# Kernel tuning notes

Hardware: AMD Instinct MI355X
Metric: run time of the kernel (lower is better)

## Reference

```python
import jax, jax.numpy as jnp
import numpy as np

EPS = 1e-6        # RMSNorm140 eps
LAM = 0.1         # lambda_: second-order score weight
HAD = 0.05        # hadamard_scale

def _rmsnorm(x, w):
    return x * jax.lax.rsqrt(jnp.mean(x * x, axis=-1, keepdims=True) + EPS) * w

def _rope(x):
    # x: [b, h, s, d]; interleaved-pair rotary embedding (theta=10000)
    b, h, s, d = x.shape
    inv = 1.0 / (10000.0 ** (jnp.arange(0, d, 2, dtype=jnp.float32) / d))
    ang = jnp.arange(s, dtype=jnp.float32)[:, None] * inv[None, :]  # [s, d/2]
    cos, sin = jnp.cos(ang), jnp.sin(ang)
    x1, x2 = x[..., 0::2], x[..., 1::2]
    out = jnp.stack([x1 * cos - x2 * sin, x1 * sin + x2 * cos], axis=-1)
    return out.reshape(b, h, s, d)

def _rotate_half(x):
    d = x.shape[-1] // 2
    return jnp.concatenate([-x[..., d:], x[..., :d]], axis=-1)

def _attn_pass(Q, K, V):
    # scores = (Q@K^T + lam * Q^2 @ (K^2)^T) / sqrt(head_dim)   (second-order amplify)
    scale = 1.0 / jnp.sqrt(jnp.float32(Q.shape[-1]))
    scores = (jnp.einsum('bhsd,bhtd->bhst', Q, K)
              + LAM * jnp.einsum('bhsd,bhtd->bhst', Q * Q, K * K)) * scale
    return jnp.einsum('bhst,bhtd->bhsd', jax.nn.softmax(scores, axis=-1), V)

def _attention(x, wq, wk, wv, wo, gate_w):
    b, s, dim = x.shape
    hd = gate_w.shape[0]
    nh = dim // hd
    def proj(w):  # StickyLinear: x @ W^T, W stored [out, in]
        return (x @ w.T).reshape(b, s, nh, hd).transpose(0, 2, 1, 3)  # [b,h,s,d]
    Q, K, V = proj(wq), proj(wk), proj(wv)
    Q, K = _rope(Q), _rope(K)
    out1 = _attn_pass(Q, K, V)
    # rotated second pass + per-channel sigmoid gate over head_dim
    out2 = _attn_pass(_rotate_half(Q), _rotate_half(K), V)
    g = jax.nn.sigmoid(gate_w)
    out = out1 * (1.0 - g) + out2 * g
    out = out + HAD * out * out  # Hadamard mix (elementwise nonlinearity)
    out = out.transpose(0, 2, 1, 3).reshape(b, s, dim)
    return out @ wo.T

def _ffn(x, w1, w3, w2):
    # SwiGLU: down( silu(gate(x)) * up(x) )
    return (jax.nn.silu(x @ w1.T) * (x @ w3.T)) @ w2.T

def reference(x, norm1_w, norm2_w, wq, wk, wv, wo, gate_w, w1, w3, w2):
    h = x + _attention(_rmsnorm(x, norm1_w), wq, wk, wv, wo, gate_w)
    return h + _ffn(_rmsnorm(h, norm2_w), w1, w3, w2)

def setup_inputs() -> dict:
    B, S, D, NH, DFF = 2, 1024, 2048, 16, 8192
    HD = D // NH
    key = jax.random.key(0)
    ks = jax.random.split(key, 9)
    std = 0.02
    return {
        'x': jax.random.normal(ks[0], (B, S, D), dtype=jnp.float32),
        'norm1_w': jnp.ones((D,), jnp.float32),
        'norm2_w': jnp.ones((D,), jnp.float32),
        'wq': jax.random.normal(ks[1], (D, D), jnp.float32) * std,
        'wk': jax.random.normal(ks[2], (D, D), jnp.float32) * std,
        'wv': jax.random.normal(ks[3], (D, D), jnp.float32) * std,
        'wo': jax.random.normal(ks[4], (D, D), jnp.float32) * std,
        'gate_w': jax.random.normal(ks[5], (HD,), jnp.float32) * 0.01,
        'w1': jax.random.normal(ks[6], (DFF, D), jnp.float32) * std,
        'w3': jax.random.normal(ks[7], (DFF, D), jnp.float32) * std,
        'w2': jax.random.normal(ks[8], (D, DFF), jnp.float32) * std,
    }
```

## Files before the change

kernel.cpp:

```cpp
#include <hip/hip_runtime.h>
#include <hip/hip_bf16.h>

typedef unsigned short u16;
typedef unsigned int u32;
typedef u16 u16x8 __attribute__((ext_vector_type(8)));
typedef float f32x4 __attribute__((ext_vector_type(4)));

__device__ __forceinline__ u16 f2bf(float f) {
  union { float f; u32 u; } v; v.f = f;
  u32 r = v.u + 0x7FFFu + ((v.u >> 16) & 1u);
  return (u16)(r >> 16);
}
__device__ __forceinline__ float bf2f(u16 h) {
  union { u32 u; float f; } v; v.u = ((u32)h) << 16;
  return v.f;
}
__device__ __forceinline__ void mfma_bf16_16x16x32(f32x4& acc, const f32x4& a, const f32x4& b) {
  asm("v_mfma_f32_16x16x32_bf16 %0, %1, %2, %0" : "+v"(acc) : "v"(a), "v"(b));
}
__device__ __forceinline__ void gload_lds16(const void* g, void* l) {
  __builtin_amdgcn_global_load_lds(
      (const __attribute__((address_space(1))) unsigned int*)g,
      (__attribute__((address_space(3))) unsigned int*)l, 16, 0, 0);
}

__global__ __launch_bounds__(256) void cvt_k(const float* __restrict__ src,
                                             u16* __restrict__ dst, int n8) {
  int i = blockIdx.x * 256 + threadIdx.x;
  if (i >= n8) return;
  float4 f0 = *(const float4*)&src[(size_t)i * 8];
  float4 f1 = *(const float4*)&src[(size_t)i * 8 + 4];
  u16x8 o;
  o[0] = f2bf(f0.x); o[1] = f2bf(f0.y); o[2] = f2bf(f0.z); o[3] = f2bf(f0.w);
  o[4] = f2bf(f1.x); o[5] = f2bf(f1.y); o[6] = f2bf(f1.z); o[7] = f2bf(f1.w);
  *(u16x8*)&dst[(size_t)i * 8] = o;
}

__global__ __launch_bounds__(256) void cvt13_k(const float* __restrict__ src,
                                               u16* __restrict__ dst, int half) {
  int r = blockIdx.x;
  int dr = ((r >> 4) << 5) + (r & 15) + (half << 4);
  int t = threadIdx.x;
  const float* s = src + (size_t)r * 2048 + t * 8;
  float4 f0 = *(const float4*)s;
  float4 f1 = *(const float4*)(s + 4);
  u16x8 o;
  o[0] = f2bf(f0.x); o[1] = f2bf(f0.y); o[2] = f2bf(f0.z); o[3] = f2bf(f0.w);
  o[4] = f2bf(f1.x); o[5] = f2bf(f1.y); o[6] = f2bf(f1.z); o[7] = f2bf(f1.w);
  *(u16x8*)&dst[(size_t)dr * 2048 + t * 8] = o;
}

__global__ __launch_bounds__(256) void rmsnorm_k(const float* __restrict__ X,
                                                 const float* __restrict__ W,
                                                 u16* __restrict__ O) {
  const int row = blockIdx.x;
  const int tid = threadIdx.x;
  const float* x = X + (size_t)row * 2048;
  float4 v0 = *(const float4*)&x[tid * 8];
  float4 v1 = *(const float4*)&x[tid * 8 + 4];
  float s = v0.x * v0.x + v0.y * v0.y + v0.z * v0.z + v0.w * v0.w
          + v1.x * v1.x + v1.y * v1.y + v1.z * v1.z + v1.w * v1.w;
  #pragma unroll
  for (int m = 1; m < 64; m <<= 1) s += __shfl_xor(s, m);
  __shared__ float red[4];
  if ((tid & 63) == 0) red[tid >> 6] = s;
  __syncthreads();
  float tot = red[0] + red[1] + red[2] + red[3];
  float r = rsqrtf(tot * (1.0f / 2048.0f) + 1e-6f);
  float4 w0 = *(const float4*)&W[tid * 8];
  float4 w1 = *(const float4*)&W[tid * 8 + 4];
  u16x8 o;
  o[0] = f2bf(v0.x * r * w0.x); o[1] = f2bf(v0.y * r * w0.y);
  o[2] = f2bf(v0.z * r * w0.z); o[3] = f2bf(v0.w * r * w0.w);
  o[4] = f2bf(v1.x * r * w1.x); o[5] = f2bf(v1.y * r * w1.y);
  o[6] = f2bf(v1.z * r * w1.z); o[7] = f2bf(v1.w * r * w1.w);
  *(u16x8*)&O[(size_t)row * 2048 + tid * 8] = o;
}

#define EPI_F32 0
#define EPI_ADDF32 1
#define EPI_SWIGLU 2

template <int EPI>
__global__ __launch_bounds__(256) void gemm_bt(const u16* __restrict__ A,
                                               const u16* __restrict__ B,
                                               float* __restrict__ Cf,
                                               u16* __restrict__ Cb,
                                               const float* __restrict__ R,
                                               int M, int N, int Kt,
                                               int lda, int ldb) {
  __shared__ __align__(16) u16 As[128 * 32];
  __shared__ __align__(16) u16 Bs[128 * 32];
  const int tid = threadIdx.x;
  const int lane = tid & 63;
  const int w = tid >> 6;
  const int wm = w >> 1, wn = w & 1;
  const int m0 = blockIdx.y * 128, n0 = blockIdx.x * 128;
  const int z = blockIdx.z;
  A += (size_t)z * Kt;
  B += (size_t)z * Kt;
  Cf += (size_t)z * M * N;
  const int r0 = tid >> 2;
  const int c0 = (tid & 3) * 8;
  const int r1 = r0 + 64;
  const int laneM = lane & 15;
  const int laneK = (lane >> 4) * 8;

  f32x4 acc[4][4];
  #pragma unroll
  for (int i = 0; i < 4; i++)
    #pragma unroll
    for (int j = 0; j < 4; j++) acc[i][j] = (f32x4){0.f, 0.f, 0.f, 0.f};

  const u16* Ar0 = &A[(size_t)(m0 + r0) * lda + c0];
  const u16* Ar1 = &A[(size_t)(m0 + r1) * lda + c0];
  const u16* Br0 = &B[(size_t)(n0 + r0) * ldb + c0];
  const u16* Br1 = &B[(size_t)(n0 + r1) * ldb + c0];
  u16* lA0 = &As[r0 * 32 + c0];
  u16* lA1 = &As[r1 * 32 + c0];
  u16* lB0 = &Bs[r0 * 32 + c0];
  u16* lB1 = &Bs[r1 * 32 + c0];

  for (int kt = 0; kt < Kt; kt += 32) {
    __syncthreads();
    gload_lds16(Ar0 + kt, lA0);
    gload_lds16(Ar1 + kt, lA1);
    gload_lds16(Br0 + kt, lB0);
    gload_lds16(Br1 + kt, lB1);
    __syncthreads();
    f32x4 af[4], bfr[4];
    #pragma unroll
    for (int mi = 0; mi < 4; mi++)
      af[mi] = *(const f32x4*)&As[(wm * 64 + mi * 16 + laneM) * 32 + laneK];
    #pragma unroll
    for (int ni = 0; ni < 4; ni++)
      bfr[ni] = *(const f32x4*)&Bs[(wn * 64 + ni * 16 + laneM) * 32 + laneK];
    #pragma unroll
    for (int mi = 0; mi < 4; mi++)
      #pragma unroll
      for (int ni = 0; ni < 4; ni++)
        mfma_bf16_16x16x32(acc[mi][ni], af[mi], bfr[ni]);
  }

  const int rowb = (lane >> 4) * 4;
  const int coll = lane & 15;
  #pragma unroll
  for (int mi = 0; mi < 4; mi++) {
    #pragma unroll
    for (int i = 0; i < 4; i++) {
      int row = m0 + wm * 64 + mi * 16 + rowb + i;
      if constexpr (EPI == EPI_SWIGLU) {
        #pragma unroll
        for (int ni = 0; ni < 4; ni += 2) {
          float g = acc[mi][ni][i];
          float u = acc[mi][ni + 1][i];
          float sg = g / (1.0f + __expf(-g));
          int j = (n0 >> 1) + wn * 32 + (ni >> 1) * 16 + coll;
          Cb[(size_t)row * (N >> 1) + j] = f2bf(sg * u);
        }
      } else {
        #pragma unroll
        for (int ni = 0; ni < 4; ni++) {
          int col = n0 + wn * 64 + ni * 16 + coll;
          size_t idx = (size_t)row * N + col;
          float v = acc[mi][ni][i];
          if constexpr (EPI == EPI_F32) Cf[idx] = v;
          else Cf[idx] = v + R[idx];
        }
      }
    }
  }
}

__global__ __launch_bounds__(256) void reduce5_k(const float* __restrict__ P,
                                                 const float* __restrict__ H,
                                                 float* __restrict__ out) {
  size_t i = ((size_t)blockIdx.x * 256 + threadIdx.x) * 4;
  const size_t MN = 4194304;
  float4 a = *(const float4*)&P[i];
  float4 b = *(const float4*)&P[MN + i];
  float4 c = *(const float4*)&P[2 * MN + i];
  float4 d = *(const float4*)&P[3 * MN + i];
  float4 h = *(const float4*)&H[i];
  float4 o;
  o.x = a.x + b.x + c.x + d.x + h.x;
  o.y = a.y + b.y + c.y + d.y + h.y;
  o.z = a.z + b.z + c.z + d.z + h.z;
  o.w = a.w + b.w + c.w + d.w + h.w;
  *(float4*)&out[i] = o;
}

__device__ __forceinline__ void rope_row(const float* __restrict__ src,
                                         u16* __restrict__ dst, int s, int q4) {
  float vv[32];
  #pragma unroll
  for (int t = 0; t < 8; t++) {
    float4 f = *(const float4*)&src[t * 4];
    vv[t * 4] = f.x; vv[t * 4 + 1] = f.y; vv[t * 4 + 2] = f.z; vv[t * 4 + 3] = f.w;
  }
  u16 o1[32], o2[32];
  #pragma unroll
  for (int jl = 0; jl < 16; jl++) {
    int j = q4 * 16 + jl;
    float inv = exp2f(-(float)j * 0.20762050593046014f);
    float ang = (float)s * inv;
    float sn, cs;
    __sincosf(ang, &sn, &cs);
    float a = vv[2 * jl], b = vv[2 * jl + 1];
    float r1 = a * cs - b * sn;
    float r2 = a * sn + b * cs;
    o1[2 * jl] = f2bf(r1);
    o1[2 * jl + 1] = f2bf(r2);
    o2[2 * jl] = f2bf(0.31622776601683794f * r1 * r1);
    o2[2 * jl + 1] = f2bf(0.31622776601683794f * r2 * r2);
  }
  #pragma unroll
  for (int t = 0; t < 4; t++) {
    *(u16x8*)&dst[q4 * 32 + t * 8] = *(const u16x8*)&o1[t * 8];
    *(u16x8*)&dst[128 + q4 * 32 + t * 8] = *(const u16x8*)&o2[t * 8];
  }
}

__global__ __launch_bounds__(256) void qkv_post_k(const float* __restrict__ QKVF,
                                                  u16* __restrict__ Qe,
                                                  u16* __restrict__ Ke,
                                                  u16* __restrict__ Vt) {
  const int st = blockIdx.x;
  const int bh = blockIdx.y;
  const int b = bh >> 4, h = bh & 15;
  const int tid = threadIdx.x;
  {
    int r = tid >> 2, q4 = tid & 3;
    int s = st * 64 + r;
    size_t rowin = ((size_t)b * 1024 + s) * 6144 + h * 128 + q4 * 32;
    size_t rowe = ((size_t)bh * 1024 + s) * 256;
    rope_row(QKVF + rowin, Qe + rowe, s, q4);
    rope_row(QKVF + rowin + 2048, Ke + rowe, s, q4);
  }
  __shared__ __align__(16) u16 vts[128 * 72];
  {
    int r = tid >> 2, q4 = tid & 3;
    int s = st * 64 + r;
    const float* src = QKVF + ((size_t)b * 1024 + s) * 6144 + 4096 + h * 128 + q4 * 32;
    #pragma unroll
    for (int k = 0; k < 32; k += 4) {
      float4 f = *(const float4*)&src[k];
      int d = q4 * 32 + k;
      vts[(d + 0) * 72 + r] = f2bf(f.x);
      vts[(d + 1) * 72 + r] = f2bf(f.y);
      vts[(d + 2) * 72 + r] = f2bf(f.z);
      vts[(d + 3) * 72 + r] = f2bf(f.w);
    }
  }
  __syncthreads();
  {
    int d = tid >> 1, sp = (tid & 1) * 32;
    u16* dst = Vt + ((size_t)bh * 128 + d) * 1024 + st * 64 + sp;
    #pragma unroll
    for (int k = 0; k < 32; k += 8)
      *(u16x8*)&dst[k] = *(const u16x8*)&vts[d * 72 + sp + k];
  }
}

__global__ __launch_bounds__(256, 2) void attn_k(const u16* __restrict__ Qe,
                                                 const u16* __restrict__ Ke,
                                                 const u16* __restrict__ Vt,
                                                 u16* __restrict__ AO) {
  const int bh = blockIdx.x;
  const int qt = blockIdx.y;
  const int b = bh >> 4, h = bh & 15;
  const int tid = threadIdx.x;
  const int w = tid >> 6, lane = tid & 63;
  const int laneM = lane & 15, laneG = lane >> 4;

  __shared__ __align__(16) char smem[57344];
  u16* plu = (u16*)(smem + 49152 + w * 2048);

  const char* KeB = (const char*)Ke + (size_t)bh * 524288;
  const char* VtB = (const char*)Vt + (size_t)bh * 262144;

  const size_t qbase = ((size_t)bh * 1024 + qt * 64 + w * 16 + laneM) * 256 + laneG * 8;
  f32x4 qf[8];
  #pragma unroll
  for (int kk = 0; kk < 8; kk++) qf[kk] = *(const f32x4*)&Qe[qbase + kk * 32];

  float m_i[4], l_i[4];
  #pragma unroll
  for (int i = 0; i < 4; i++) { m_i[i] = -1e30f; l_i[i] = 0.f; }
  f32x4 accO[8];
  #pragma unroll
  for (int n = 0; n < 8; n++) accO[n] = (f32x4){0.f, 0.f, 0.f, 0.f};

  u16x8 kreg[4], vreg[2];
  auto loadRegs = [&](int ktn) {
    const char* ks = KeB + (size_t)ktn * 16384;
    #pragma unroll
    for (int j = 0; j < 4; j++) {
      int p = j * 4096 + tid * 16;
      kreg[j] = *(const u16x8*)(ks + p);
    }
    const char* vs = VtB + (size_t)ktn * 64;
    #pragma unroll
    for (int j = 0; j < 2; j++) {
      int p = j * 4096 + tid * 16;
      int r = p >> 6, x = p & 63;
      vreg[j] = *(const u16x8*)(vs + (size_t)r * 2048 + x);
    }
  };
  auto writeLDS = [&](int bsel) {
    char* kd = smem + (bsel ? 16384 : 0);
    #pragma unroll
    for (int j = 0; j < 4; j++) {
      int p = j * 4096 + tid * 16;
      int r = p >> 9, x = p & 511;
      *(u16x8*)(kd + r * 512 + (x ^ ((r & 7) << 4))) = kreg[j];
    }
    char* vd = smem + 32768 + (bsel ? 8192 : 0);
    #pragma unroll
    for (int j = 0; j < 2; j++) {
      int p = j * 4096 + tid * 16;
      int r = p >> 6, x = p & 63;
      *(u16x8*)(vd + r * 64 + (x ^ (((r >> 1) & 3) << 4))) = vreg[j];
    }
  };

  loadRegs(0);
  writeLDS(0);
  int cur = 0;
  const float scale = 0.08838834764831845f;

  for (int kt = 0; kt < 32; kt++) {
    if (kt < 31) loadRegs(kt + 1);
    __syncthreads();
    const char* Kc = smem + (cur ? 16384 : 0);
    const char* Vc = smem + 32768 + (cur ? 8192 : 0);

    f32x4 accS[2];
    #pragma unroll
    for (int n = 0; n < 2; n++) accS[n] = (f32x4){0.f, 0.f, 0.f, 0.f};
    #pragma unroll
    for (int n = 0; n < 2; n++) {
      int r = n * 16 + laneM;
      const char* krow = Kc + r * 512;
      int sw = (r & 7) << 4;
      #pragma unroll
      for (int kk = 0; kk < 8; kk++) {
        f32x4 kf = *(const f32x4*)(krow + ((kk * 64 + laneG * 16) ^ sw));
        mfma_bf16_16x16x32(accS[n], qf[kk], kf);
      }
    }

    float p[2][4], sf[4];
    #pragma unroll
    for (int i = 0; i < 4; i++) {
      float mx = fmaxf(accS[0][i], accS[1][i]) * scale;
      #pragma unroll
      for (int m = 1; m < 16; m <<= 1) mx = fmaxf(mx, __shfl_xor(mx, m));
      float mnew = fmaxf(m_i[i], mx);
      sf[i] = __expf(m_i[i] - mnew);
      m_i[i] = mnew;
      float p0 = __expf(accS[0][i] * scale - mnew);
      float p1 = __expf(accS[1][i] * scale - mnew);
      p[0][i] = p0; p[1][i] = p1;
      float rs = p0 + p1;
      #pragma unroll
      for (int m = 1; m < 16; m <<= 1) rs += __shfl_xor(rs, m);
      l_i[i] = l_i[i] * sf[i] + rs;
    }
    #pragma unroll
    for (int n = 0; n < 8; n++) {
      accO[n][0] *= sf[0]; accO[n][1] *= sf[1];
      accO[n][2] *= sf[2]; accO[n][3] *= sf[3];
    }

    #pragma unroll
    for (int n = 0; n < 2; n++)
      #pragma unroll
      for (int i = 0; i < 4; i++) {
        int row = laneG * 4 + i;
        int col = n * 16 + laneM;
        plu[row * 64 + (col ^ (((row >> 2) & 3) << 4))] = f2bf(p[n][i]);
      }
    f32x4 pa = *(const f32x4*)&plu[laneM * 64 +
                                   ((laneG * 8) ^ (((laneM >> 2) & 3) << 4))];

    #pragma unroll
    for (int n = 0; n < 8; n++) {
      int r = n * 16 + laneM;
      f32x4 vf = *(const f32x4*)(Vc + r * 64 + ((laneG * 16) ^ (((r >> 1) & 3) << 4)));
      mfma_bf16_16x16x32(accO[n], pa, vf);
    }

    if (kt < 31) writeLDS(cur ^ 1);
    cur ^= 1;
  }

  #pragma unroll
  for (int i = 0; i < 4; i++) {
    float inv_l = 1.f / l_i[i];
    int row = b * 1024 + qt * 64 + w * 16 + laneG * 4 + i;
    #pragma unroll
    for (int n = 0; n < 8; n++) {
      float o = accO[n][i] * inv_l;
      o = o + 0.05f * o * o;
      AO[(size_t)row * 2048 + h * 128 + n * 16 + laneM] = f2bf(o);
    }
  }
}

extern "C" void kernel_launch(void* const* d_in, const int* in_sizes, int n_in,
                              void* d_out, int out_size, void* d_ws, size_t ws_size,
                              hipStream_t stream) {
  const float* x   = (const float*)d_in[0];
  const float* n1w = (const float*)d_in[1];
  const float* n2w = (const float*)d_in[2];
  const float* wq  = (const float*)d_in[3];
  const float* wk  = (const float*)d_in[4];
  const float* wv  = (const float*)d_in[5];
  const float* wo  = (const float*)d_in[6];
  const float* w1  = (const float*)d_in[8];
  const float* w3  = (const float*)d_in[9];
  const float* w2  = (const float*)d_in[10];

  char* ws = (char*)d_ws;
  u16* WQKVb = (u16*)(ws + 0);
  u16* WOb   = (u16*)(ws + 25165824);
  u16* W13b  = (u16*)(ws + 33554432);
  u16* W2b   = (u16*)(ws + 100663296);
  u16* XN    = (u16*)(ws + 134217728);
  float* QKVF = (float*)(ws + 142606336);
  u16* U     = (u16*)(ws + 142606336);
  float* P   = (float*)(ws + 176160768);
  u16* QE    = (u16*)(ws + 192937984);
  u16* KE    = (u16*)(ws + 209715200);
  u16* VT    = (u16*)(ws + 226492416);
  u16* AO    = (u16*)(ws + 234881024);
  float* H   = (float*)(ws + 243269632);

  cvt_k<<<2048, 256, 0, stream>>>(wq, WQKVb, 524288);
  cvt_k<<<2048, 256, 0, stream>>>(wk, WQKVb + 4194304, 524288);
  cvt_k<<<2048, 256, 0, stream>>>(wv, WQKVb + 8388608, 524288);
  cvt_k<<<2048, 256, 0, stream>>>(wo, WOb, 524288);
  cvt13_k<<<8192, 256, 0, stream>>>(w1, W13b, 0);
  cvt13_k<<<8192, 256, 0, stream>>>(w3, W13b, 1);
  cvt_k<<<8192, 256, 0, stream>>>(w2, W2b, 2097152);

  rmsnorm_k<<<2048, 256, 0, stream>>>(x, n1w, XN);

  gemm_bt<EPI_F32><<<dim3(48, 16), 256, 0, stream>>>(
      XN, WQKVb, QKVF, nullptr, nullptr, 2048, 6144, 2048, 2048, 2048);

  qkv_post_k<<<dim3(16, 32), 256, 0, stream>>>(QKVF, QE, KE, VT);

  attn_k<<<dim3(32, 16), 256, 0, stream>>>(QE, KE, VT, AO);

  gemm_bt<EPI_ADDF32><<<dim3(16, 16), 256, 0, stream>>>(
      AO, WOb, H, nullptr, x, 2048, 2048, 2048, 2048, 2048);

  rmsnorm_k<<<2048, 256, 0, stream>>>(H, n2w, XN);

  gemm_bt<EPI_SWIGLU><<<dim3(128, 16), 256, 0, stream>>>(
      XN, W13b, nullptr, U, nullptr, 2048, 16384, 2048, 2048, 2048);

  gemm_bt<EPI_F32><<<dim3(16, 16, 4), 256, 0, stream>>>(
      U, W2b, P, nullptr, nullptr, 2048, 2048, 2048, 8192, 8192);

  reduce5_k<<<4096, 256, 0, stream>>>(P, H, (float*)d_out);
}
```

Measured before the change: 565.9 us.

## Double-buffer GEMM LDS tiles to overlap global loads with MFMA

Converts the bf16 GEMM main loop from single-buffered LDS staging to a two-stage ping-pong buffer. The next K-tile's global-to-LDS loads are issued before computing on the current tile, with explicit vmcnt waits and barriers replacing the two __syncthreads per iteration. This aims to hide global memory latency behind MFMA work, at the cost of doubling LDS use per block (32KB), which may reduce occupancy.

After: 568.7 us. About the same (+0.5%).

```diff
diff --git a/kernel.cpp b/kernel.cpp
--- a/kernel.cpp
+++ b/kernel.cpp
@@ -89,8 +89,8 @@
                                                const float* __restrict__ R,
                                                int M, int N, int Kt,
                                                int lda, int ldb) {
-  __shared__ __align__(16) u16 As[128 * 32];
-  __shared__ __align__(16) u16 Bs[128 * 32];
+  __shared__ __align__(16) u16 As[2][128 * 32];
+  __shared__ __align__(16) u16 Bs[2][128 * 32];
   const int tid = threadIdx.x;
   const int lane = tid & 63;
   const int w = tid >> 6;
@@ -116,30 +116,42 @@
   const u16* Ar1 = &A[(size_t)(m0 + r1) * lda + c0];
   const u16* Br0 = &B[(size_t)(n0 + r0) * ldb + c0];
   const u16* Br1 = &B[(size_t)(n0 + r1) * ldb + c0];
-  u16* lA0 = &As[r0 * 32 + c0];
-  u16* lA1 = &As[r1 * 32 + c0];
-  u16* lB0 = &Bs[r0 * 32 + c0];
-  u16* lB1 = &Bs[r1 * 32 + c0];
-
-  for (int kt = 0; kt < Kt; kt += 32) {
-    __syncthreads();
-    gload_lds16(Ar0 + kt, lA0);
-    gload_lds16(Ar1 + kt, lA1);
-    gload_lds16(Br0 + kt, lB0);
-    gload_lds16(Br1 + kt, lB1);
-    __syncthreads();
+  const int lofs0 = r0 * 32 + c0;
+  const int lofs1 = r1 * 32 + c0;
+
+  auto stage = [&](int bsel, int kt) {
+    gload_lds16(Ar0 + kt, &As[bsel][lofs0]);
+    gload_lds16(Ar1 + kt, &As[bsel][lofs1]);
+    gload_lds16(Br0 + kt, &Bs[bsel][lofs0]);
+    gload_lds16(Br1 + kt, &Bs[bsel][lofs1]);
+  };
+
+  stage(0, 0);
+  const int nt = Kt >> 5;
+  for (int t = 0; t < nt; t++) {
+    const int cur = t & 1;
+    if (t + 1 < nt) {
+      stage(cur ^ 1, (t + 1) << 5);
+      asm volatile("s_waitcnt vmcnt(4)" ::: "memory");
+    } else {
+      asm volatile("s_waitcnt vmcnt(0)" ::: "memory");
+    }
+    __builtin_amdgcn_s_barrier();
+    __builtin_amdgcn_sched_barrier(0);
     f32x4 af[4], bfr[4];
     #pragma unroll
     for (int mi = 0; mi < 4; mi++)
-      af[mi] = *(const f32x4*)&As[(wm * 64 + mi * 16 + laneM) * 32 + laneK];
+      af[mi] = *(const f32x4*)&As[cur][(wm * 64 + mi * 16 + laneM) * 32 + laneK];
     #pragma unroll
     for (int ni = 0; ni < 4; ni++)
-      bfr[ni] = *(const f32x4*)&Bs[(wn * 64 + ni * 16 + laneM) * 32 + laneK];
+      bfr[ni] = *(const f32x4*)&Bs[cur][(wn * 64 + ni * 16 + laneM) * 32 + laneK];
     #pragma unroll
     for (int mi = 0; mi < 4; mi++)
       #pragma unroll
       for (int ni = 0; ni < 4; ni++)
         mfma_bf16_16x16x32(acc[mi][ni], af[mi], bfr[ni]);
+    __builtin_amdgcn_sched_barrier(0);
+    __builtin_amdgcn_s_barrier();
   }
 
   const int rowb = (lane >> 4) * 4;
```
